# Kernel optimization log

Hardware: AMD Instinct MI355X
Metric: run time of the kernel (lower is better)

The kernel has to match this reference:

```python
import jax, jax.numpy as jnp
import numpy as np

DIM = 512
HEADS = 8
DIM_HEAD = 64
HIDDEN = HEADS * DIM_HEAD  # 512
B, N = 16, 4096
EPS = 1e-5


def setup_inputs() -> dict:
    key = jax.random.key(0)
    k1, k2, k3 = jax.random.split(key, 3)
    x = jax.random.normal(k1, (B, DIM, N), dtype=jnp.float32)
    # Conv1d kernel-size-1 weights stored as [out_ch, in_ch]
    w_qkv = jax.random.normal(k2, (3 * HIDDEN, DIM), dtype=jnp.float32) / np.sqrt(DIM)
    w_out = jax.random.normal(k3, (DIM, HIDDEN), dtype=jnp.float32) / np.sqrt(HIDDEN)
    b_out = jnp.zeros((DIM,), dtype=jnp.float32)
    g_out = jnp.ones((DIM,), dtype=jnp.float32)  # channel LayerNorm gamma
    return {"x": x, "w_qkv": w_qkv, "w_out": w_out, "b_out": b_out, "g_out": g_out}


def reference(x, w_qkv, w_out, b_out, g_out):
    b, c, n = x.shape
    scale = DIM_HEAD ** (-0.5)
    # 1x1 conv projection to q,k,v: [b, 3*hidden, n]
    qkv = jnp.einsum('bcn,oc->bon', x, w_qkv)
    q, k, v = jnp.split(qkv, 3, axis=1)
    rs = lambda t: t.reshape(b, HEADS, DIM_HEAD, n)  # b (m d) n -> b m d n
    q, k, v = rs(q), rs(k), rs(v)
    q = jax.nn.softmax(q, axis=2) * scale  # softmax over head-dim d
    k = jax.nn.softmax(k, axis=3)          # softmax over sequence n
    # context: k v^T outer-product summed over sequence -> [b, m, d, d]
    context = jnp.einsum('bmin,bmjn->bmij', k, v)
    # apply context to queries -> [b, m, d, n]
    out = jnp.einsum('bmij,bmin->bmjn', context, q)
    out = out.reshape(b, HIDDEN, n)  # b m d n -> b (m d) n
    # output 1x1 conv with bias
    out = jnp.einsum('bcn,oc->bon', out, w_out) + b_out[None, :, None]
    # channel LayerNorm (gamma-only, biased variance over channel axis)
    mean = out.mean(axis=1, keepdims=True)
    var = out.var(axis=1, keepdims=True)
    return (out - mean) * jax.lax.rsqrt(var + EPS) * g_out[None, :, None]
```

## Files before the change

kernel.cpp:

```cpp
#include <hip/hip_runtime.h>

#define NB 16
#define CDIM 512
#define NHEAD 8
#define DHEAD 64
#define NSEQ 4096
#define O3 1536

typedef __attribute__((ext_vector_type(8))) short short8;
typedef __attribute__((ext_vector_type(4))) float f32x4;
typedef __attribute__((ext_vector_type(4))) unsigned u32x4;
typedef __attribute__((ext_vector_type(2))) unsigned u32x2;
typedef __attribute__((ext_vector_type(4))) float fvec4;

__device__ __forceinline__ float bf2f(unsigned short u){
  union { unsigned u; float f; } v; v.u = ((unsigned)u) << 16; return v.f;
}
__device__ __forceinline__ unsigned short f2bf(float f){
  union { float f; unsigned u; } v; v.f = f;
  unsigned r = v.u + 0x7fffu + ((v.u >> 16) & 1u);
  return (unsigned short)(r >> 16);
}
__device__ __forceinline__ unsigned pack2(float a, float b){
  return (unsigned)f2bf(a) | ((unsigned)f2bf(b) << 16);
}
__device__ __forceinline__ void gld_lds16(const void* g, void* l){
  __builtin_amdgcn_global_load_lds(
      (const __attribute__((address_space(1))) unsigned*)g,
      (__attribute__((address_space(3))) unsigned*)l, 16, 0, 0);
}

__global__ __launch_bounds__(256) void k_conv_w(const float* __restrict__ w,
                                                unsigned short* __restrict__ o){
  int i = (blockIdx.x*256 + threadIdx.x)*4;
  fvec4 v = *(const fvec4*)(w + i);
  u32x2 p; p[0] = pack2(v[0], v[1]); p[1] = pack2(v[2], v[3]);
  *(u32x2*)(o + i) = p;
}

__global__ __launch_bounds__(256) void k_transpose_x(const float* __restrict__ x,
                                                     unsigned short* __restrict__ xT){
  __shared__ unsigned short tile[64][65];
  int b = blockIdx.z, c0 = blockIdx.y*64, n0 = blockIdx.x*64;
  int t = threadIdx.x;
  const float* xb = x + ((size_t)b*CDIM + c0)*NSEQ + n0;
  #pragma unroll
  for (int i=0;i<4;i++){
    int idx = t + i*256;
    int r = idx>>4, c4 = (idx&15)*4;
    fvec4 v = *(const fvec4*)(xb + (size_t)r*NSEQ + c4);
    tile[r][c4]   = f2bf(v[0]);
    tile[r][c4+1] = f2bf(v[1]);
    tile[r][c4+2] = f2bf(v[2]);
    tile[r][c4+3] = f2bf(v[3]);
  }
  __syncthreads();
  unsigned short* ob = xT + ((size_t)b*NSEQ + n0)*CDIM + c0;
  #pragma unroll
  for (int i=0;i<4;i++){
    int idx = t + i*256;
    int r = idx>>4, c4 = (idx&15)*4;
    u32x2 p;
    p[0] = (unsigned)tile[c4][r]   | ((unsigned)tile[c4+1][r] << 16);
    p[1] = (unsigned)tile[c4+2][r] | ((unsigned)tile[c4+3][r] << 16);
    *(u32x2*)(ob + (size_t)r*CDIM + c4) = p;
  }
}

__global__ __launch_bounds__(256) void k_gemm_qkv(const unsigned short* __restrict__ A,
                                                  const unsigned short* __restrict__ Bt,
                                                  unsigned short* __restrict__ KV,
                                                  unsigned short* __restrict__ qsmT){
  __shared__ unsigned short smem[128*128];
  unsigned short* As = smem;
  unsigned short* Bs = smem + 4096;
  int b = blockIdx.z;
  int n0 = blockIdx.x*128, o0 = blockIdx.y*128;
  const unsigned short* Bb = Bt + (size_t)b*NSEQ*CDIM;
  int t = threadIdx.x, w = t>>6, l = t&63;
  int lr = l&15, kq = (l>>4)*8;
  int wr = (w>>1)*64, wc = (w&1)*64;
  f32x4 acc[4][4];
  #pragma unroll
  for (int mi=0;mi<4;mi++)
    #pragma unroll
    for (int ni=0;ni<4;ni++) acc[mi][ni] = (f32x4){0.f,0.f,0.f,0.f};
  for (int k0=0;k0<CDIM;k0+=32){
    #pragma unroll
    for (int it=0;it<2;++it){
      int chunk = it*256 + t;
      int row = chunk>>2, kc = (chunk&3)*8;
      gld_lds16(A  + (size_t)(o0+row)*CDIM + k0 + kc, (char*)As + (size_t)(it*256+w*64)*16);
      gld_lds16(Bb + (size_t)(n0+row)*CDIM + k0 + kc, (char*)Bs + (size_t)(it*256+w*64)*16);
    }
    __syncthreads();
    short8 af[4], bfv[4];
    #pragma unroll
    for (int mi=0;mi<4;mi++) af[mi]  = *(const short8*)&As[(wr + mi*16 + lr)*32 + kq];
    #pragma unroll
    for (int ni=0;ni<4;ni++) bfv[ni] = *(const short8*)&Bs[(wc + ni*16 + lr)*32 + kq];
    #pragma unroll
    for (int mi=0;mi<4;mi++)
      #pragma unroll
      for (int ni=0;ni<4;ni++)
        acc[mi][ni] = __builtin_amdgcn_mfma_f32_16x16x32_bf16(af[mi], bfv[ni], acc[mi][ni], 0, 0, 0);
    __syncthreads();
  }
  if (o0 < 512){
    __syncthreads();
    unsigned short* tile = smem;
    #pragma unroll
    for (int mi=0;mi<4;mi++)
      #pragma unroll
      for (int ni=0;ni<4;ni++)
        #pragma unroll
        for (int r=0;r<4;r++){
          int row = wr + mi*16 + (l>>4)*4 + r;
          int col = wc + ni*16 + lr;
          tile[row*128 + col] = f2bf(acc[mi][ni][r]);
        }
    __syncthreads();
    int col = t & 127, h = t >> 7;
    const unsigned short* cptr = &tile[(h*64)*128 + col];
    float mx = -1e30f;
    #pragma unroll
    for (int d=0; d<64; ++d) mx = fmaxf(mx, bf2f(cptr[d*128]));
    float sm = 0.f;
    #pragma unroll
    for (int d=0; d<64; ++d) sm += __expf(bf2f(cptr[d*128]) - mx);
    float inv = 0.125f / sm;
    unsigned* dst = (unsigned*)(qsmT + ((size_t)b*NSEQ + n0 + col)*CDIM + (size_t)(o0 + h*64));
    #pragma unroll
    for (int d=0; d<64; d+=2){
      float a0 = __expf(bf2f(cptr[d*128])     - mx) * inv;
      float a1 = __expf(bf2f(cptr[(d+1)*128]) - mx) * inv;
      dst[d>>1] = pack2(a0, a1);
    }
  } else {
    unsigned short* Cb = KV + (size_t)b*1024*NSEQ;
    int ob = o0 - 512;
    #pragma unroll
    for (int mi=0;mi<4;mi++)
      #pragma unroll
      for (int ni=0;ni<4;ni++)
        #pragma unroll
        for (int r=0;r<4;r++){
          int row = ob + wr + mi*16 + (l>>4)*4 + r;
          int col = n0 + wc + ni*16 + lr;
          Cb[(size_t)row*NSEQ + col] = f2bf(acc[mi][ni][r]);
        }
  }
}

__global__ __launch_bounds__(256) void k_kstats(const unsigned short* __restrict__ KV,
                                                float* __restrict__ kmax, float* __restrict__ ksum){
  int w = threadIdx.x>>6, l = threadIdx.x&63;
  int idx = blockIdx.x*4 + w;
  int b = idx>>9, row = idx&511;
  const unsigned short* kp = KV + ((size_t)b*1024 + row)*NSEQ;
  u32x4 kv[8];
  #pragma unroll
  for (int it=0;it<8;++it) kv[it] = ((const u32x4*)kp)[it*64 + l];
  float mx = -1e30f;
  #pragma unroll
  for (int it=0;it<8;++it)
    #pragma unroll
    for (int c=0;c<4;++c){
      unsigned u = kv[it][c];
      mx = fmaxf(mx, fmaxf(bf2f((unsigned short)u), bf2f((unsigned short)(u>>16))));
    }
  #pragma unroll
  for (int s=1;s<64;s<<=1) mx = fmaxf(mx, __shfl_xor(mx, s, 64));
  float sm = 0.f;
  #pragma unroll
  for (int it=0;it<8;++it)
    #pragma unroll
    for (int c=0;c<4;++c){
      unsigned u = kv[it][c];
      sm += __expf(bf2f((unsigned short)u) - mx) + __expf(bf2f((unsigned short)(u>>16)) - mx);
    }
  #pragma unroll
  for (int s=1;s<64;s<<=1) sm += __shfl_xor(sm, s, 64);
  if (l == 0){ kmax[idx] = mx; ksum[idx] = sm; }
}

__global__ __launch_bounds__(256) void k_context(const unsigned short* __restrict__ KV,
                                                 const float* __restrict__ kmax,
                                                 const float* __restrict__ ksum,
                                                 float* __restrict__ ctx4){
  __shared__ unsigned short Vs[64*64];
  int m = blockIdx.x, b = blockIdx.y, ch = blockIdx.z;
  int t = threadIdx.x, w = t>>6, l = t&63;
  int lr = l&15, kq = (l>>4)*8;
  const unsigned short* kbase = KV + ((size_t)b*1024 + m*64)*NSEQ;
  const unsigned short* vbase = KV + ((size_t)b*1024 + 512 + m*64)*NSEQ;
  int irow = w*16 + lr;
  float rmax = kmax[b*512 + m*64 + irow];
  f32x4 acc[4];
  #pragma unroll
  for (int jf=0;jf<4;++jf) acc[jf] = (f32x4){0.f,0.f,0.f,0.f};
  int nbeg = ch*1024, nend = nbeg + 1024;
  for (int n0=nbeg;n0<nend;n0+=64){
    #pragma unroll
    for (int it=0;it<2;++it){
      int chunk = it*256 + t;
      int row = chunk>>3, kc = (chunk&7)*8;
      gld_lds16(vbase + (size_t)row*NSEQ + n0 + kc, (char*)Vs + (size_t)(it*256+w*64)*16);
    }
    __syncthreads();
    #pragma unroll
    for (int kk=0;kk<2;++kk){
      u32x4 kraw = *(const u32x4*)(kbase + (size_t)irow*NSEQ + n0 + kk*32 + kq);
      short8 af;
      #pragma unroll
      for (int c=0;c<4;++c){
        unsigned u = kraw[c];
        float f0 = __expf(bf2f((unsigned short)u) - rmax);
        float f1 = __expf(bf2f((unsigned short)(u>>16)) - rmax);
        af[c*2]   = (short)f2bf(f0);
        af[c*2+1] = (short)f2bf(f1);
      }
      #pragma unroll
      for (int jf=0;jf<4;++jf){
        short8 bv = *(const short8*)&Vs[(jf*16+lr)*64 + kk*32 + kq];
        acc[jf] = __builtin_amdgcn_mfma_f32_16x16x32_bf16(af, bv, acc[jf], 0, 0, 0);
      }
    }
    __syncthreads();
  }
  float* cb = ctx4 + (((size_t)ch*NB + b)*NHEAD + m)*4096;
  #pragma unroll
  for (int jf=0;jf<4;++jf)
    #pragma unroll
    for (int r=0;r<4;++r){
      int i = w*16 + (l>>4)*4 + r;
      int j = jf*16 + lr;
      cb[i*64 + j] = acc[jf][r] / ksum[b*512 + m*64 + i];
    }
}

__global__ __launch_bounds__(256) void k_weff(const float* __restrict__ ctx4,
                                              const float* __restrict__ wout,
                                              unsigned short* __restrict__ weff){
  __shared__ float cs[64][65];
  int m = blockIdx.x, b = blockIdx.y;
  int t = threadIdx.x, w = t>>6, l = t&63;
  const float* cb = ctx4 + ((size_t)b*NHEAD + m)*4096;
  const size_t chs = (size_t)NB*NHEAD*4096;
  for (int idx=t; idx<4096; idx+=256)
    cs[idx>>6][idx&63] = cb[idx] + cb[idx+chs] + cb[idx+2*chs] + cb[idx+3*chs];
  __syncthreads();
  for (int oo=0;oo<128;++oo){
    int o = w*128 + oo;
    float acc = 0.f;
    #pragma unroll
    for (int j=0;j<64;++j) acc += wout[(size_t)o*CDIM + m*64 + j] * cs[l][j];
    weff[((size_t)b*CDIM + o)*CDIM + m*64 + l] = f2bf(acc);
  }
}

__global__ __launch_bounds__(512) void k_out_ln(const unsigned short* __restrict__ Weff,
                                                const unsigned short* __restrict__ QT,
                                                const float* __restrict__ bias,
                                                const float* __restrict__ g,
                                                float* __restrict__ out){
  __shared__ unsigned short As[512*32];
  __shared__ unsigned short Bs[64*32];
  __shared__ float lnS[64], lnS2[64];
  int b = blockIdx.y, n0 = blockIdx.x*64;
  const unsigned short* Ab = Weff + (size_t)b*CDIM*CDIM;
  const unsigned short* Bb = QT + ((size_t)b*NSEQ + n0)*CDIM;
  int t = threadIdx.x, w = t>>6, l = t&63;
  int lr = l&15, kq = (l>>4)*8;
  f32x4 acc[4][4];
  #pragma unroll
  for (int mi=0;mi<4;mi++)
    #pragma unroll
    for (int ni=0;ni<4;ni++) acc[mi][ni] = (f32x4){0.f,0.f,0.f,0.f};
  for (int k0=0;k0<CDIM;k0+=32){
    #pragma unroll
    for (int it=0;it<4;++it){
      int chunk = it*512 + t;
      int row = chunk>>2, kc = (chunk&3)*8;
      gld_lds16(Ab + (size_t)row*CDIM + k0 + kc, (char*)As + (size_t)chunk*16);
    }
    if (t < 256){
      int row = t>>2, kc = (t&3)*8;
      gld_lds16(Bb + (size_t)row*CDIM + k0 + kc, (char*)Bs + (size_t)t*16);
    }
    __syncthreads();
    short8 af[4], bfv[4];
    #pragma unroll
    for (int mi=0;mi<4;mi++) af[mi]  = *(const short8*)&As[(w*64 + mi*16 + lr)*32 + kq];
    #pragma unroll
    for (int ni=0;ni<4;ni++) bfv[ni] = *(const short8*)&Bs[(ni*16 + lr)*32 + kq];
    #pragma unroll
    for (int mi=0;mi<4;mi++)
      #pragma unroll
      for (int ni=0;ni<4;ni++)
        acc[mi][ni] = __builtin_amdgcn_mfma_f32_16x16x32_bf16(af[mi], bfv[ni], acc[mi][ni], 0, 0, 0);
    __syncthreads();
  }
  if (t < 64){ lnS[t] = 0.f; lnS2[t] = 0.f; }
  __syncthreads();
  float ps[4], ps2[4];
  #pragma unroll
  for (int ni=0;ni<4;ni++){ ps[ni]=0.f; ps2[ni]=0.f; }
  #pragma unroll
  for (int mi=0;mi<4;mi++)
    #pragma unroll
    for (int r=0;r<4;r++){
      int row = w*64 + mi*16 + (l>>4)*4 + r;
      float bb = bias[row];
      #pragma unroll
      for (int ni=0;ni<4;ni++){
        float v = acc[mi][ni][r] + bb;
        acc[mi][ni][r] = v;
        ps[ni] += v; ps2[ni] += v*v;
      }
    }
  #pragma unroll
  for (int ni=0;ni<4;ni++){
    ps[ni]  += __shfl_xor(ps[ni], 16, 64);  ps[ni]  += __shfl_xor(ps[ni], 32, 64);
    ps2[ni] += __shfl_xor(ps2[ni], 16, 64); ps2[ni] += __shfl_xor(ps2[ni], 32, 64);
  }
  if ((l>>4) == 0){
    #pragma unroll
    for (int ni=0;ni<4;ni++){
      atomicAdd(&lnS[ni*16+lr],  ps[ni]);
      atomicAdd(&lnS2[ni*16+lr], ps2[ni]);
    }
  }
  __syncthreads();
  if (t < 64){
    float mean = lnS[t]*(1.f/512.f);
    float var  = lnS2[t]*(1.f/512.f) - mean*mean;
    lnS[t] = mean; lnS2[t] = rsqrtf(var + 1e-5f);
  }
  __syncthreads();
  float* ob = out + (size_t)b*CDIM*NSEQ + n0;
  #pragma unroll
  for (int ni=0;ni<4;ni++){
    int col = ni*16 + lr;
    float mean = lnS[col], rstd = lnS2[col];
    #pragma unroll
    for (int mi=0;mi<4;mi++)
      #pragma unroll
      for (int r=0;r<4;r++){
        int row = w*64 + mi*16 + (l>>4)*4 + r;
        ob[(size_t)row*NSEQ + col] = (acc[mi][ni][r] - mean)*rstd*g[row];
      }
  }
}

extern "C" void kernel_launch(void* const* d_in, const int* in_sizes, int n_in,
                              void* d_out, int out_size, void* d_ws, size_t ws_size,
                              hipStream_t stream){
  const float* x     = (const float*)d_in[0];
  const float* w_qkv = (const float*)d_in[1];
  const float* w_out = (const float*)d_in[2];
  const float* b_out = (const float*)d_in[3];
  const float* g_out = (const float*)d_in[4];
  float* out = (float*)d_out;
  char* ws = (char*)d_ws;

  size_t off = 0;
  unsigned short* wq_bf = (unsigned short*)(ws + off); off += (size_t)O3*CDIM*2;
  char* xT_region = ws + off;                          off += (size_t)NB*NSEQ*CDIM*2;
  unsigned short* qkv_kv = (unsigned short*)(ws + off); off += (size_t)NB*1024*NSEQ*2;
  unsigned short* qsmT   = (unsigned short*)(ws + off); off += (size_t)NB*NSEQ*CDIM*2;
  if (off > ws_size) return;
  unsigned short* xT = (unsigned short*)xT_region;
  float* kmaxp = (float*)(xT_region);
  float* ksump = (float*)(xT_region + (64<<10));
  float* ctx4  = (float*)(xT_region + (1<<20));
  unsigned short* weff = (unsigned short*)(xT_region + (16<<20));

  k_conv_w     <<<O3*CDIM/1024, 256, 0, stream>>>(w_qkv, wq_bf);
  k_transpose_x<<<dim3(NSEQ/64, CDIM/64, NB), 256, 0, stream>>>(x, xT);
  k_gemm_qkv   <<<dim3(NSEQ/128, O3/128, NB), 256, 0, stream>>>(wq_bf, xT, qkv_kv, qsmT);
  k_kstats     <<<NB*CDIM/4, 256, 0, stream>>>(qkv_kv, kmaxp, ksump);
  k_context    <<<dim3(NHEAD, NB, 4), 256, 0, stream>>>(qkv_kv, kmaxp, ksump, ctx4);
  k_weff       <<<dim3(NHEAD, NB), 256, 0, stream>>>(ctx4, w_out, weff);
  k_out_ln     <<<dim3(NSEQ/64, NB), 512, 0, stream>>>(weff, qsmT, b_out, g_out, out);
}
```

Measured before the change: 440.8 us.

## Split QKV GEMM, register-level q softmax, widen out-LN tile, parallelize weff

The fused QKV GEMM is split into a K/V GEMM with small LDS tiles and a Q GEMM that computes the head-dim softmax in registers using cross-lane shuffles. Results are then staged through a padded LDS tile so they can be written with coalesced stores, replacing the earlier bf16 round trip and column-serial softmax. The out-projection+LayerNorm kernel doubles its sequence tile to 128 columns, raising reuse of the weight tile at the cost of more accumulator registers. The weff kernel adds a z-dimension so four times as many blocks share the work. LDS-async destination addressing is also simplified to chunk*16.

```diff
diff --git a/kernel.cpp b/kernel.cpp
--- a/kernel.cpp
+++ b/kernel.cpp
@@ -67,11 +67,61 @@
   }
 }
 
-__global__ __launch_bounds__(256) void k_gemm_qkv(const unsigned short* __restrict__ A,
-                                                  const unsigned short* __restrict__ Bt,
-                                                  unsigned short* __restrict__ KV,
-                                                  unsigned short* __restrict__ qsmT){
-  __shared__ unsigned short smem[128*128];
+__global__ __launch_bounds__(256) void k_gemm_kv(const unsigned short* __restrict__ A,
+                                                 const unsigned short* __restrict__ Bt,
+                                                 unsigned short* __restrict__ KV){
+  __shared__ unsigned short As[128*32];
+  __shared__ unsigned short Bs[128*32];
+  int b = blockIdx.z;
+  int n0 = blockIdx.x*128, o0 = blockIdx.y*128;
+  const unsigned short* Bb = Bt + (size_t)b*NSEQ*CDIM;
+  unsigned short* Cb = KV + (size_t)b*1024*NSEQ;
+  int t = threadIdx.x, w = t>>6, l = t&63;
+  int lr = l&15, kq = (l>>4)*8;
+  int wr = (w>>1)*64, wc = (w&1)*64;
+  f32x4 acc[4][4];
+  #pragma unroll
+  for (int mi=0;mi<4;mi++)
+    #pragma unroll
+    for (int ni=0;ni<4;ni++) acc[mi][ni] = (f32x4){0.f,0.f,0.f,0.f};
+  for (int k0=0;k0<CDIM;k0+=32){
+    #pragma unroll
+    for (int it=0;it<2;++it){
+      int chunk = it*256 + t;
+      int row = chunk>>2, kc = (chunk&3)*8;
+      gld_lds16(A  + (size_t)(o0+row)*CDIM + k0 + kc, (char*)As + (size_t)chunk*16);
+      gld_lds16(Bb + (size_t)(n0+row)*CDIM + k0 + kc, (char*)Bs + (size_t)chunk*16);
+    }
+    __syncthreads();
+    short8 af[4], bfv[4];
+    #pragma unroll
+    for (int mi=0;mi<4;mi++) af[mi]  = *(const short8*)&As[(wr + mi*16 + lr)*32 + kq];
+    #pragma unroll
+    for (int ni=0;ni<4;ni++) bfv[ni] = *(const short8*)&Bs[(wc + ni*16 + lr)*32 + kq];
+    #pragma unroll
+    for (int mi=0;mi<4;mi++)
+      #pragma unroll
+      for (int ni=0;ni<4;ni++)
+        acc[mi][ni] = __builtin_amdgcn_mfma_f32_16x16x32_bf16(af[mi], bfv[ni], acc[mi][ni], 0, 0, 0);
+    __syncthreads();
+  }
+  #pragma unroll
+  for (int mi=0;mi<4;mi++)
+    #pragma unroll
+    for (int ni=0;ni<4;ni++)
+      #pragma unroll
+      for (int r=0;r<4;r++){
+        int row = o0 + wr + mi*16 + (l>>4)*4 + r;
+        int col = n0 + wc + ni*16 + lr;
+        Cb[(size_t)row*NSEQ + col] = f2bf(acc[mi][ni][r]);
+      }
+}
+
+#define TS 136
+__global__ __launch_bounds__(256) void k_gemm_q(const unsigned short* __restrict__ A,
+                                                const unsigned short* __restrict__ Bt,
+                                                unsigned short* __restrict__ qsmT){
+  __shared__ unsigned short smem[64*TS];
   unsigned short* As = smem;
   unsigned short* Bs = smem + 4096;
   int b = blockIdx.z;
@@ -90,8 +140,8 @@
     for (int it=0;it<2;++it){
       int chunk = it*256 + t;
       int row = chunk>>2, kc = (chunk&3)*8;
-      gld_lds16(A  + (size_t)(o0+row)*CDIM + k0 + kc, (char*)As + (size_t)(it*256+w*64)*16);
-      gld_lds16(Bb + (size_t)(n0+row)*CDIM + k0 + kc, (char*)Bs + (size_t)(it*256+w*64)*16);
+      gld_lds16(A  + (size_t)(o0+row)*CDIM + k0 + kc, (char*)As + (size_t)chunk*16);
+      gld_lds16(Bb + (size_t)(n0+row)*CDIM + k0 + kc, (char*)Bs + (size_t)chunk*16);
     }
     __syncthreads();
     short8 af[4], bfv[4];
@@ -106,49 +156,52 @@
         acc[mi][ni] = __builtin_amdgcn_mfma_f32_16x16x32_bf16(af[mi], bfv[ni], acc[mi][ni], 0, 0, 0);
     __syncthreads();
   }
-  if (o0 < 512){
-    __syncthreads();
-    unsigned short* tile = smem;
-    #pragma unroll
-    for (int mi=0;mi<4;mi++)
-      #pragma unroll
-      for (int ni=0;ni<4;ni++)
+  unsigned pk[4][4][2];
+  #pragma unroll
+  for (int ni=0;ni<4;ni++){
+    float mx = -1e30f;
+    #pragma unroll
+    for (int mi=0;mi<4;mi++)
+      #pragma unroll
+      for (int r=0;r<4;r++) mx = fmaxf(mx, acc[mi][ni][r]);
+    mx = fmaxf(mx, __shfl_xor(mx, 16, 64));
+    mx = fmaxf(mx, __shfl_xor(mx, 32, 64));
+    float s = 0.f;
+    #pragma unroll
+    for (int mi=0;mi<4;mi++)
+      #pragma unroll
+      for (int r=0;r<4;r++){
+        float p = __expf(acc[mi][ni][r] - mx);
+        acc[mi][ni][r] = p; s += p;
+      }
+    s += __shfl_xor(s, 16, 64);
+    s += __shfl_xor(s, 32, 64);
+    float inv = 0.125f / s;
+    #pragma unroll
+    for (int mi=0;mi<4;mi++){
+      pk[mi][ni][0] = pack2(acc[mi][ni][0]*inv, acc[mi][ni][1]*inv);
+      pk[mi][ni][1] = pack2(acc[mi][ni][2]*inv, acc[mi][ni][3]*inv);
+    }
+  }
+  #pragma unroll
+  for (int ck=0;ck<2;++ck){
+    if ((w&1) == ck){
+      #pragma unroll
+      for (int mi=0;mi<4;mi++)
         #pragma unroll
-        for (int r=0;r<4;r++){
-          int row = wr + mi*16 + (l>>4)*4 + r;
-          int col = wc + ni*16 + lr;
-          tile[row*128 + col] = f2bf(acc[mi][ni][r]);
+        for (int ni=0;ni<4;ni++){
+          int idx = (ni*16 + lr)*TS + wr + mi*16 + (l>>4)*4;
+          u32x2 p; p[0] = pk[mi][ni][0]; p[1] = pk[mi][ni][1];
+          *(u32x2*)&smem[idx] = p;
         }
-    __syncthreads();
-    int col = t & 127, h = t >> 7;
-    const unsigned short* cptr = &tile[(h*64)*128 + col];
-    float mx = -1e30f;
-    #pragma unroll
-    for (int d=0; d<64; ++d) mx = fmaxf(mx, bf2f(cptr[d*128]));
-    float sm = 0.f;
-    #pragma unroll
-    for (int d=0; d<64; ++d) sm += __expf(bf2f(cptr[d*128]) - mx);
-    float inv = 0.125f / sm;
-    unsigned* dst = (unsigned*)(qsmT + ((size_t)b*NSEQ + n0 + col)*CDIM + (size_t)(o0 + h*64));
-    #pragma unroll
-    for (int d=0; d<64; d+=2){
-      float a0 = __expf(bf2f(cptr[d*128])     - mx) * inv;
-      float a1 = __expf(bf2f(cptr[(d+1)*128]) - mx) * inv;
-      dst[d>>1] = pack2(a0, a1);
-    }
-  } else {
-    unsigned short* Cb = KV + (size_t)b*1024*NSEQ;
-    int ob = o0 - 512;
-    #pragma unroll
-    for (int mi=0;mi<4;mi++)
-      #pragma unroll
-      for (int ni=0;ni<4;ni++)
-        #pragma unroll
-        for (int r=0;r<4;r++){
-          int row = ob + wr + mi*16 + (l>>4)*4 + r;
-          int col = n0 + wc + ni*16 + lr;
-          Cb[(size_t)row*NSEQ + col] = f2bf(acc[mi][ni][r]);
-        }
+    }
+    __syncthreads();
+    int col = t>>2, rs = (t&3)*32;
+    unsigned short* dst = qsmT + ((size_t)b*NSEQ + n0 + ck*64 + col)*CDIM + o0 + rs;
+    #pragma unroll
+    for (int j=0;j<4;++j)
+      *(u32x4*)(dst + j*8) = *(const u32x4*)&smem[col*TS + rs + j*8];
+    __syncthreads();
   }
 }
 
@@ -205,7 +258,7 @@
     for (int it=0;it<2;++it){
       int chunk = it*256 + t;
       int row = chunk>>3, kc = (chunk&7)*8;
-      gld_lds16(vbase + (size_t)row*NSEQ + n0 + kc, (char*)Vs + (size_t)(it*256+w*64)*16);
+      gld_lds16(vbase + (size_t)row*NSEQ + n0 + kc, (char*)Vs + (size_t)chunk*16);
     }
     __syncthreads();
     #pragma unroll
@@ -243,15 +296,15 @@
                                               const float* __restrict__ wout,
                                               unsigned short* __restrict__ weff){
   __shared__ float cs[64][65];
-  int m = blockIdx.x, b = blockIdx.y;
+  int m = blockIdx.x, b = blockIdx.y, z = blockIdx.z;
   int t = threadIdx.x, w = t>>6, l = t&63;
   const float* cb = ctx4 + ((size_t)b*NHEAD + m)*4096;
   const size_t chs = (size_t)NB*NHEAD*4096;
   for (int idx=t; idx<4096; idx+=256)
     cs[idx>>6][idx&63] = cb[idx] + cb[idx+chs] + cb[idx+2*chs] + cb[idx+3*chs];
   __syncthreads();
-  for (int oo=0;oo<128;++oo){
-    int o = w*128 + oo;
+  for (int oo=0;oo<32;++oo){
+    int o = z*128 + w*32 + oo;
     float acc = 0.f;
     #pragma unroll
     for (int j=0;j<64;++j) acc += wout[(size_t)o*CDIM + m*64 + j] * cs[l][j];
@@ -265,18 +318,18 @@
                                                 const float* __restrict__ g,
                                                 float* __restrict__ out){
   __shared__ unsigned short As[512*32];
-  __shared__ unsigned short Bs[64*32];
-  __shared__ float lnS[64], lnS2[64];
-  int b = blockIdx.y, n0 = blockIdx.x*64;
+  __shared__ unsigned short Bs[128*32];
+  __shared__ float lnS[128], lnS2[128];
+  int b = blockIdx.y, n0 = blockIdx.x*128;
   const unsigned short* Ab = Weff + (size_t)b*CDIM*CDIM;
   const unsigned short* Bb = QT + ((size_t)b*NSEQ + n0)*CDIM;
   int t = threadIdx.x, w = t>>6, l = t&63;
   int lr = l&15, kq = (l>>4)*8;
-  f32x4 acc[4][4];
+  f32x4 acc[4][8];
   #pragma unroll
   for (int mi=0;mi<4;mi++)
     #pragma unroll
-    for (int ni=0;ni<4;ni++) acc[mi][ni] = (f32x4){0.f,0.f,0.f,0.f};
+    for (int ni=0;ni<8;ni++) acc[mi][ni] = (f32x4){0.f,0.f,0.f,0.f};
   for (int k0=0;k0<CDIM;k0+=32){
     #pragma unroll
     for (int it=0;it<4;++it){
@@ -284,28 +337,28 @@
       int row = chunk>>2, kc = (chunk&3)*8;
       gld_lds16(Ab + (size_t)row*CDIM + k0 + kc, (char*)As + (size_t)chunk*16);
     }
-    if (t < 256){
+    {
       int row = t>>2, kc = (t&3)*8;
       gld_lds16(Bb + (size_t)row*CDIM + k0 + kc, (char*)Bs + (size_t)t*16);
     }
     __syncthreads();
-    short8 af[4], bfv[4];
+    short8 af[4], bfv[8];
     #pragma unroll
     for (int mi=0;mi<4;mi++) af[mi]  = *(const short8*)&As[(w*64 + mi*16 + lr)*32 + kq];
     #pragma unroll
-    for (int ni=0;ni<4;ni++) bfv[ni] = *(const short8*)&Bs[(ni*16 + lr)*32 + kq];
-    #pragma unroll
-    for (int mi=0;mi<4;mi++)
-      #pragma unroll
-      for (int ni=0;ni<4;ni++)
+    for (int ni=0;ni<8;ni++) bfv[ni] = *(const short8*)&Bs[(ni*16 + lr)*32 + kq];
+    #pragma unroll
+    for (int mi=0;mi<4;mi++)
+      #pragma unroll
+      for (int ni=0;ni<8;ni++)
         acc[mi][ni] = __builtin_amdgcn_mfma_f32_16x16x32_bf16(af[mi], bfv[ni], acc[mi][ni], 0, 0, 0);
     __syncthreads();
   }
-  if (t < 64){ lnS[t] = 0.f; lnS2[t] = 0.f; }
+  if (t < 128){ lnS[t] = 0.f; lnS2[t] = 0.f; }
   __syncthreads();
-  float ps[4], ps2[4];
-  #pragma unroll
-  for (int ni=0;ni<4;ni++){ ps[ni]=0.f; ps2[ni]=0.f; }
+  float ps[8], ps2[8];
+  #pragma unroll
+  for (int ni=0;ni<8;ni++){ ps[ni]=0.f; ps2[ni]=0.f; }
   #pragma unroll
   for (int mi=0;mi<4;mi++)
     #pragma unroll
@@ -313,26 +366,26 @@
       int row = w*64 + mi*16 + (l>>4)*4 + r;
       float bb = bias[row];
       #pragma unroll
-      for (int ni=0;ni<4;ni++){
+      for (int ni=0;ni<8;ni++){
         float v = acc[mi][ni][r] + bb;
         acc[mi][ni][r] = v;
         ps[ni] += v; ps2[ni] += v*v;
       }
     }
   #pragma unroll
-  for (int ni=0;ni<4;ni++){
+  for (int ni=0;ni<8;ni++){
     ps[ni]  += __shfl_xor(ps[ni], 16, 64);  ps[ni]  += __shfl_xor(ps[ni], 32, 64);
     ps2[ni] += __shfl_xor(ps2[ni], 16, 64); ps2[ni] += __shfl_xor(ps2[ni], 32, 64);
   }
   if ((l>>4) == 0){
     #pragma unroll
-    for (int ni=0;ni<4;ni++){
+    for (int ni=0;ni<8;ni++){
       atomicAdd(&lnS[ni*16+lr],  ps[ni]);
       atomicAdd(&lnS2[ni*16+lr], ps2[ni]);
     }
   }
   __syncthreads();
-  if (t < 64){
+  if (t < 128){
     float mean = lnS[t]*(1.f/512.f);
     float var  = lnS2[t]*(1.f/512.f) - mean*mean;
     lnS[t] = mean; lnS2[t] = rsqrtf(var + 1e-5f);
@@ -340,7 +393,7 @@
   __syncthreads();
   float* ob = out + (size_t)b*CDIM*NSEQ + n0;
   #pragma unroll
-  for (int ni=0;ni<4;ni++){
+  for (int ni=0;ni<8;ni++){
     int col = ni*16 + lr;
     float mean = lnS[col], rstd = lnS2[col];
     #pragma unroll
@@ -378,9 +431,10 @@
 
   k_conv_w     <<<O3*CDIM/1024, 256, 0, stream>>>(w_qkv, wq_bf);
   k_transpose_x<<<dim3(NSEQ/64, CDIM/64, NB), 256, 0, stream>>>(x, xT);
-  k_gemm_qkv   <<<dim3(NSEQ/128, O3/128, NB), 256, 0, stream>>>(wq_bf, xT, qkv_kv, qsmT);
+  k_gemm_kv    <<<dim3(NSEQ/128, 8, NB), 256, 0, stream>>>(wq_bf + (size_t)512*CDIM, xT, qkv_kv);
+  k_gemm_q     <<<dim3(NSEQ/128, 4, NB), 256, 0, stream>>>(wq_bf, xT, qsmT);
   k_kstats     <<<NB*CDIM/4, 256, 0, stream>>>(qkv_kv, kmaxp, ksump);
   k_context    <<<dim3(NHEAD, NB, 4), 256, 0, stream>>>(qkv_kv, kmaxp, ksump, ctx4);
-  k_weff       <<<dim3(NHEAD, NB), 256, 0, stream>>>(ctx4, w_out, weff);
-  k_out_ln     <<<dim3(NSEQ/64, NB), 512, 0, stream>>>(weff, qsmT, b_out, g_out, out);
-}
+  k_weff       <<<dim3(NHEAD, NB, 4), 256, 0, stream>>>(ctx4, w_out, weff);
+  k_out_ln     <<<dim3(NSEQ/128, NB), 512, 0, stream>>>(weff, qsmT, b_out, g_out, out);
+}
```

New measurement: 380.8 us. 1.16x faster.
